# Kernel optimization log

Measured on AMD Instinct MI355X. Metric: run time of the kernel, lower is better.

The kernel has to match this reference:

```python
import jax, jax.numpy as jnp
import numpy as np

EPS = 1e-12  # torch F.normalize eps

def _l2norm(v, axis):
    n = jnp.sqrt(jnp.sum(v * v, axis=axis, keepdims=True))
    return v / jnp.maximum(n, EPS)

def setup_inputs() -> dict:
    key = jax.random.key(0)
    ks = jax.random.split(key, 5)
    B, N, C, K = 16, 512, 384, 64
    return {
        "x": jax.random.normal(ks[0], (B, N, C), dtype=jnp.float32),
        "centers": jax.random.normal(ks[1], (C, K), dtype=jnp.float32),
        "tran_ms": jax.random.normal(ks[2], (K, N, N), dtype=jnp.float32),
        "proj_w": jax.random.normal(ks[3], (C, C), dtype=jnp.float32) * 0.02,
        "proj_b": jax.random.normal(ks[4], (C,), dtype=jnp.float32) * 0.02,
    }

def reference(x, centers, tran_ms, proj_w, proj_b):
    # x: [B,N,C]
    q = x.mean(axis=1)                              # [B,C] mean-pooled query
    qn = _l2norm(q, axis=-1)                        # F.normalize(q, dim=-1)
    cn = _l2norm(centers, axis=0)                   # F.normalize(centers, dim=0)
    attn = jax.nn.softmax(qn @ cn, axis=-1)         # [B,K] cluster routing weights
    # combine transition matrices: equivalent to the (B,K,N,N) repeat/sum,
    # expressed as a single contraction producing [B,N,N]
    tm = jnp.einsum('bk,knm->bnm', attn, tran_ms)   # [B,N,N]
    y = jnp.einsum('bnm,bmc->bnc', tm, x)           # bmm
    out = y @ proj_w.T + proj_b                     # nn.Linear(dim, dim)
    return out
```

## Files before the change

### kernel.cpp

```cpp
#include <hip/hip_runtime.h>
#include <math.h>
#include <stdint.h>

#define B_  16
#define N_  512
#define C_  384
#define K_  64
#define NN_ (N_*N_)

typedef short bf16x8 __attribute__((ext_vector_type(8)));
typedef float f32x4  __attribute__((ext_vector_type(4)));

__device__ __forceinline__ unsigned short f2bf(float f) {
    union { float f; unsigned u; } v; v.f = f;
    unsigned r = v.u + 0x7FFF + ((v.u >> 16) & 1);
    return (unsigned short)(r >> 16);
}

__device__ __forceinline__ void gl_lds16(const void* g, void* l) {
    __builtin_amdgcn_global_load_lds(
        (const __attribute__((address_space(1))) unsigned*)g,
        (__attribute__((address_space(3))) unsigned*)l, 16, 0, 0);
}

__global__ __launch_bounds__(384) void mean_kernel(const float* __restrict__ x,
                                                   float* __restrict__ q,
                                                   unsigned short* __restrict__ xb) {
    const int b = blockIdx.y;
    const int s = blockIdx.x;
    const int c = threadIdx.x;
    const size_t base = ((size_t)(b * N_ + s * 16)) * C_ + c;
    const float* xp = x + base;
    unsigned short* xo = xb + base;
    float acc = 0.f;
#pragma unroll
    for (int i = 0; i < 16; ++i) {
        float v = xp[(size_t)i * C_];
        acc += v;
        xo[(size_t)i * C_] = f2bf(v);
    }
    atomicAdd(&q[b * C_ + c], acc);
}

__global__ __launch_bounds__(256) void wconv_kernel(const float* __restrict__ w,
                                                    unsigned short* __restrict__ wb) {
    const int i = (blockIdx.x * 256 + threadIdx.x) * 4;
    const float4 v = *(const float4*)(w + i);
    unsigned u0 = ((unsigned)f2bf(v.y) << 16) | f2bf(v.x);
    unsigned u1 = ((unsigned)f2bf(v.w) << 16) | f2bf(v.z);
    *(uint2*)(wb + i) = make_uint2(u0, u1);
}

__global__ __launch_bounds__(64) void attn_kernel(const float* __restrict__ q,
                                                  const float* __restrict__ centers,
                                                  float* __restrict__ attn) {
    const int b = blockIdx.x;
    const int k = threadIdx.x;
    const float* qb = q + b * C_;

    float qn2 = 0.f;
    for (int c = k; c < C_; c += 64) { float v = qb[c]; qn2 += v * v; }
#pragma unroll
    for (int off = 32; off > 0; off >>= 1) qn2 += __shfl_xor(qn2, off);
    const float qnorm = fmaxf(sqrtf(qn2), 1e-12f);

    float dot = 0.f, cn2 = 0.f;
    for (int c = 0; c < C_; ++c) {
        float sv = centers[c * K_ + k];
        float qc = qb[c];
        dot = fmaf(qc, sv, dot);
        cn2 = fmaf(sv, sv, cn2);
    }
    const float logit = dot / (qnorm * fmaxf(sqrtf(cn2), 1e-12f));

    float m = logit;
#pragma unroll
    for (int off = 32; off > 0; off >>= 1) m = fmaxf(m, __shfl_xor(m, off));
    const float e = expf(logit - m);
    float ssum = e;
#pragma unroll
    for (int off = 32; off > 0; off >>= 1) ssum += __shfl_xor(ssum, off);
    attn[b * K_ + k] = e / ssum;
}

__global__ __launch_bounds__(256) void tm_kernel(const float* __restrict__ tran,
                                                 const float* __restrict__ attn,
                                                 unsigned short* __restrict__ tmb) {
    __shared__ float a_s[B_ * K_];
    const int tid = threadIdx.x;
    for (int i = tid; i < B_ * K_; i += 256) a_s[i] = attn[i];
    __syncthreads();

    const size_t j = ((size_t)blockIdx.x * 256 + tid) * 4;
    float4 acc[B_];
#pragma unroll
    for (int b = 0; b < B_; ++b) acc[b] = make_float4(0.f, 0.f, 0.f, 0.f);

    for (int k = 0; k < K_; ++k) {
        const float4 t = *(const float4*)(tran + (size_t)k * NN_ + j);
#pragma unroll
        for (int b = 0; b < B_; ++b) {
            float s = a_s[b * K_ + k];
            acc[b].x = fmaf(s, t.x, acc[b].x);
            acc[b].y = fmaf(s, t.y, acc[b].y);
            acc[b].z = fmaf(s, t.z, acc[b].z);
            acc[b].w = fmaf(s, t.w, acc[b].w);
        }
    }
#pragma unroll
    for (int b = 0; b < B_; ++b) {
        unsigned u0 = ((unsigned)f2bf(acc[b].y) << 16) | f2bf(acc[b].x);
        unsigned u1 = ((unsigned)f2bf(acc[b].w) << 16) | f2bf(acc[b].z);
        *(uint2*)(tmb + (size_t)b * NN_ + j) = make_uint2(u0, u1);
    }
}

__global__ __launch_bounds__(256) void xw_mfma(const unsigned short* __restrict__ Xb,
                                               const unsigned short* __restrict__ Wb,
                                               unsigned short* __restrict__ xwT) {
    __shared__ unsigned short As[64 * 64];
    __shared__ unsigned short Bs[64 * 64];
    __shared__ float T[4][32 * 35];

    const int tid  = threadIdx.x;
    const int row0 = blockIdx.x * 64;
    const int col0 = blockIdx.y * 64;
    const int lane = tid & 63;
    const int w    = tid >> 6;
    const int wm   = w & 1, wn = w >> 1;
    const int quad = lane >> 4, l15 = lane & 15;

    const int sm = tid >> 3;
    const int sc = tid & 7;

    f32x4 acc[2][2] = {};

    for (int k0 = 0; k0 < C_; k0 += 64) {
        __syncthreads();
#pragma unroll
        for (int p = 0; p < 2; ++p) {
            const int m  = p * 32 + sm;
            const int gc = sc ^ (m & 7);
            gl_lds16(Xb + (size_t)(row0 + m) * C_ + k0 + gc * 8,
                     As + (p * 256 + tid) * 8);
            gl_lds16(Wb + (size_t)(col0 + m) * C_ + k0 + gc * 8,
                     Bs + (p * 256 + tid) * 8);
        }
        __syncthreads();
#pragma unroll
        for (int kk = 0; kk < 2; ++kk) {
            bf16x8 afr[2], bfr[2];
#pragma unroll
            for (int mt = 0; mt < 2; ++mt) {
                const int mr = wm * 32 + mt * 16 + l15;
                const int kc = (kk * 4 + quad) ^ (mr & 7);
                afr[mt] = *(const bf16x8*)(As + mr * 64 + kc * 8);
            }
#pragma unroll
            for (int nt = 0; nt < 2; ++nt) {
                const int nr = wn * 32 + nt * 16 + l15;
                const int kc = (kk * 4 + quad) ^ (nr & 7);
                bfr[nt] = *(const bf16x8*)(Bs + nr * 64 + kc * 8);
            }
#pragma unroll
            for (int mt = 0; mt < 2; ++mt)
#pragma unroll
                for (int nt = 0; nt < 2; ++nt)
                    acc[mt][nt] = __builtin_amdgcn_mfma_f32_16x16x32_bf16(
                        afr[mt], bfr[nt], acc[mt][nt], 0, 0, 0);
        }
    }

#pragma unroll
    for (int mt = 0; mt < 2; ++mt)
#pragma unroll
        for (int nt = 0; nt < 2; ++nt)
#pragma unroll
            for (int r = 0; r < 4; ++r) {
                const int lrow = mt * 16 + quad * 4 + r;
                const int lcol = nt * 16 + l15;
                T[w][lrow * 35 + lcol] = acc[mt][nt][r];
            }
    __syncthreads();

    const int rw = row0 + wm * 32;
    const int b  = rw >> 9;
    const int m0 = rw & 511;
    const int c0 = col0 + wn * 32;
    unsigned short* dst = xwT + (size_t)b * C_ * N_;
#pragma unroll
    for (int i = 0; i < 8; ++i) {
        const int cl = i * 4 + quad;
        const int ml = l15 * 2;
        const float v0 = T[w][(ml + 0) * 35 + cl];
        const float v1 = T[w][(ml + 1) * 35 + cl];
        const unsigned u = ((unsigned)f2bf(v1) << 16) | f2bf(v0);
        *(unsigned*)(dst + (size_t)(c0 + cl) * N_ + m0 + ml) = u;
    }
}

__global__ __launch_bounds__(256) void out_mfma(const unsigned short* __restrict__ Ab,
                                                const unsigned short* __restrict__ Bt,
                                                const float* __restrict__ bias,
                                                float* __restrict__ out) {
    __shared__ unsigned short As[64 * 64];
    __shared__ unsigned short Bs[64 * 64];

    const int tid  = threadIdx.x;
    const int b    = blockIdx.z;
    const int row0 = blockIdx.x * 64;
    const int col0 = blockIdx.y * 64;
    const int lane = tid & 63;
    const int w    = tid >> 6;
    const int wm   = w & 1, wn = w >> 1;
    const int quad = lane >> 4, l15 = lane & 15;

    const unsigned short* Abase = Ab + (size_t)b * N_ * N_;
    const unsigned short* Bbase = Bt + (size_t)b * C_ * N_;

    const int sm = tid >> 3;
    const int sc = tid & 7;

    f32x4 acc[2][2] = {};

    for (int k0 = 0; k0 < N_; k0 += 64) {
        __syncthreads();
#pragma unroll
        for (int p = 0; p < 2; ++p) {
            const int m  = p * 32 + sm;
            const int gc = sc ^ (m & 7);
            gl_lds16(Abase + (size_t)(row0 + m) * N_ + k0 + gc * 8,
                     As + (p * 256 + tid) * 8);
            gl_lds16(Bbase + (size_t)(col0 + m) * N_ + k0 + gc * 8,
                     Bs + (p * 256 + tid) * 8);
        }
        __syncthreads();
#pragma unroll
        for (int kk = 0; kk < 2; ++kk) {
            bf16x8 afr[2], bfr[2];
#pragma unroll
            for (int mt = 0; mt < 2; ++mt) {
                const int mr = wm * 32 + mt * 16 + l15;
                const int kc = (kk * 4 + quad) ^ (mr & 7);
                afr[mt] = *(const bf16x8*)(As + mr * 64 + kc * 8);
            }
#pragma unroll
            for (int nt = 0; nt < 2; ++nt) {
                const int nr = wn * 32 + nt * 16 + l15;
                const int kc = (kk * 4 + quad) ^ (nr & 7);
                bfr[nt] = *(const bf16x8*)(Bs + nr * 64 + kc * 8);
            }
#pragma unroll
            for (int mt = 0; mt < 2; ++mt)
#pragma unroll
                for (int nt = 0; nt < 2; ++nt)
                    acc[mt][nt] = __builtin_amdgcn_mfma_f32_16x16x32_bf16(
                        afr[mt], bfr[nt], acc[mt][nt], 0, 0, 0);
        }
    }

#pragma unroll
    for (int nt = 0; nt < 2; ++nt) {
        const int c  = col0 + wn * 32 + nt * 16 + l15;
        const float bv = bias[c];
#pragma unroll
        for (int mt = 0; mt < 2; ++mt) {
            const int rbase = row0 + wm * 32 + mt * 16 + quad * 4;
#pragma unroll
            for (int r = 0; r < 4; ++r)
                out[((size_t)(b * N_ + rbase + r)) * C_ + c] = acc[mt][nt][r] + bv;
        }
    }
}

extern "C" void kernel_launch(void* const* d_in, const int* in_sizes, int n_in,
                              void* d_out, int out_size, void* d_ws, size_t ws_size,
                              hipStream_t stream) {
    const float* x       = (const float*)d_in[0];
    const float* centers = (const float*)d_in[1];
    const float* tran    = (const float*)d_in[2];
    const float* proj_w  = (const float*)d_in[3];
    const float* proj_b  = (const float*)d_in[4];
    float* out = (float*)d_out;

    float* ws   = (float*)d_ws;
    float* q    = ws;
    float* attn = ws + 6144;
    unsigned short* tmb = (unsigned short*)(ws + 8192);
    unsigned short* xwT = tmb + (size_t)B_ * N_ * N_;
    unsigned short* xb  = xwT + (size_t)B_ * C_ * N_;
    unsigned short* wb  = xb  + (size_t)B_ * N_ * C_;

    hipMemsetAsync(q, 0, (size_t)B_ * C_ * sizeof(float), stream);

    mean_kernel<<<dim3(32, 16), 384, 0, stream>>>(x, q, xb);
    wconv_kernel<<<144, 256, 0, stream>>>(proj_w, wb);
    attn_kernel<<<16, 64, 0, stream>>>(q, centers, attn);
    tm_kernel<<<256, 256, 0, stream>>>(tran, attn, tmb);
    xw_mfma<<<dim3(128, 6), 256, 0, stream>>>(xb, wb, xwT);
    out_mfma<<<dim3(8, 6, 16), 256, 0, stream>>>(tmb, xwT, proj_b, out);
}
```

Before: 158.9 us.

## Drop memset and weight-convert launches; deterministic mean partials; vectorize tm weights

Replaces atomic accumulation of the mean with per-slice partial sums that attn_kernel reduces itself, which removes the memset launch and the atomics. Removes wconv_kernel by converting proj_w to bf16 inside xw_mfma during staging, using register loads and LDS stores in place of the async global-to-LDS copy. Transposes the attention weights in LDS so tm_kernel reads four weights per float4 load. Fewer launches cut fixed overhead, but xw_mfma now reads fp32 weights repeatedly and converts them per tile.

```diff
diff --git a/kernel.cpp b/kernel.cpp
--- a/kernel.cpp
+++ b/kernel.cpp
@@ -16,6 +16,9 @@
     unsigned r = v.u + 0x7FFF + ((v.u >> 16) & 1);
     return (unsigned short)(r >> 16);
 }
+__device__ __forceinline__ unsigned pack2(float a, float b) {
+    return ((unsigned)f2bf(b) << 16) | f2bf(a);
+}
 
 __device__ __forceinline__ void gl_lds16(const void* g, void* l) {
     __builtin_amdgcn_global_load_lds(
@@ -23,8 +26,15 @@
         (__attribute__((address_space(3))) unsigned*)l, 16, 0, 0);
 }
 
+__device__ __forceinline__ void fma4(float4& c, float s, const float4& v) {
+    c.x = fmaf(s, v.x, c.x);
+    c.y = fmaf(s, v.y, c.y);
+    c.z = fmaf(s, v.z, c.z);
+    c.w = fmaf(s, v.w, c.w);
+}
+
 __global__ __launch_bounds__(384) void mean_kernel(const float* __restrict__ x,
-                                                   float* __restrict__ q,
+                                                   float* __restrict__ part,
                                                    unsigned short* __restrict__ xb) {
     const int b = blockIdx.y;
     const int s = blockIdx.x;
@@ -39,56 +49,60 @@
         acc += v;
         xo[(size_t)i * C_] = f2bf(v);
     }
-    atomicAdd(&q[b * C_ + c], acc);
-}
-
-__global__ __launch_bounds__(256) void wconv_kernel(const float* __restrict__ w,
-                                                    unsigned short* __restrict__ wb) {
-    const int i = (blockIdx.x * 256 + threadIdx.x) * 4;
-    const float4 v = *(const float4*)(w + i);
-    unsigned u0 = ((unsigned)f2bf(v.y) << 16) | f2bf(v.x);
-    unsigned u1 = ((unsigned)f2bf(v.w) << 16) | f2bf(v.z);
-    *(uint2*)(wb + i) = make_uint2(u0, u1);
-}
-
-__global__ __launch_bounds__(64) void attn_kernel(const float* __restrict__ q,
-                                                  const float* __restrict__ centers,
-                                                  float* __restrict__ attn) {
+    part[((size_t)b * 32 + s) * C_ + c] = acc;
+}
+
+__global__ __launch_bounds__(384) void attn_kernel(const float* __restrict__ part,
+                                                   const float* __restrict__ centers,
+                                                   float* __restrict__ attn) {
+    __shared__ float q_lds[C_];
+    __shared__ float red[6];
     const int b = blockIdx.x;
-    const int k = threadIdx.x;
-    const float* qb = q + b * C_;
-
-    float qn2 = 0.f;
-    for (int c = k; c < C_; c += 64) { float v = qb[c]; qn2 += v * v; }
-#pragma unroll
-    for (int off = 32; off > 0; off >>= 1) qn2 += __shfl_xor(qn2, off);
-    const float qnorm = fmaxf(sqrtf(qn2), 1e-12f);
-
-    float dot = 0.f, cn2 = 0.f;
-    for (int c = 0; c < C_; ++c) {
-        float sv = centers[c * K_ + k];
-        float qc = qb[c];
-        dot = fmaf(qc, sv, dot);
-        cn2 = fmaf(sv, sv, cn2);
-    }
-    const float logit = dot / (qnorm * fmaxf(sqrtf(cn2), 1e-12f));
-
-    float m = logit;
-#pragma unroll
-    for (int off = 32; off > 0; off >>= 1) m = fmaxf(m, __shfl_xor(m, off));
-    const float e = expf(logit - m);
-    float ssum = e;
-#pragma unroll
-    for (int off = 32; off > 0; off >>= 1) ssum += __shfl_xor(ssum, off);
-    attn[b * K_ + k] = e / ssum;
+    const int tid = threadIdx.x;
+
+    const float* pb = part + (size_t)b * 32 * C_ + tid;
+    float s = 0.f;
+#pragma unroll
+    for (int i = 0; i < 32; ++i) s += pb[(size_t)i * C_];
+    q_lds[tid] = s;
+    float p2 = s * s;
+#pragma unroll
+    for (int off = 32; off > 0; off >>= 1) p2 += __shfl_xor(p2, off);
+    if ((tid & 63) == 0) red[tid >> 6] = p2;
+    __syncthreads();
+
+    if (tid < 64) {
+        const int k = tid;
+        const float qn2 = red[0] + red[1] + red[2] + red[3] + red[4] + red[5];
+        const float qnorm = fmaxf(sqrtf(qn2), 1e-12f);
+
+        float dot = 0.f, cn2 = 0.f;
+        for (int c = 0; c < C_; ++c) {
+            float sv = centers[c * K_ + k];
+            float qc = q_lds[c];
+            dot = fmaf(qc, sv, dot);
+            cn2 = fmaf(sv, sv, cn2);
+        }
+        const float logit = dot / (qnorm * fmaxf(sqrtf(cn2), 1e-12f));
+
+        float m = logit;
+#pragma unroll
+        for (int off = 32; off > 0; off >>= 1) m = fmaxf(m, __shfl_xor(m, off));
+        const float e = expf(logit - m);
+        float ssum = e;
+#pragma unroll
+        for (int off = 32; off > 0; off >>= 1) ssum += __shfl_xor(ssum, off);
+        attn[b * K_ + k] = e / ssum;
+    }
 }
 
 __global__ __launch_bounds__(256) void tm_kernel(const float* __restrict__ tran,
                                                  const float* __restrict__ attn,
                                                  unsigned short* __restrict__ tmb) {
-    __shared__ float a_s[B_ * K_];
+    __shared__ float a_s[K_ * B_];
     const int tid = threadIdx.x;
-    for (int i = tid; i < B_ * K_; i += 256) a_s[i] = attn[i];
+    for (int i = tid; i < K_ * B_; i += 256)
+        a_s[i] = attn[(i & 15) * K_ + (i >> 4)];
     __syncthreads();
 
     const size_t j = ((size_t)blockIdx.x * 256 + tid) * 4;
@@ -98,25 +112,26 @@
 
     for (int k = 0; k < K_; ++k) {
         const float4 t = *(const float4*)(tran + (size_t)k * NN_ + j);
-#pragma unroll
-        for (int b = 0; b < B_; ++b) {
-            float s = a_s[b * K_ + k];
-            acc[b].x = fmaf(s, t.x, acc[b].x);
-            acc[b].y = fmaf(s, t.y, acc[b].y);
-            acc[b].z = fmaf(s, t.z, acc[b].z);
-            acc[b].w = fmaf(s, t.w, acc[b].w);
-        }
+        const float4* wp = (const float4*)(a_s + k * 16);
+        const float4 w0 = wp[0], w1 = wp[1], w2 = wp[2], w3 = wp[3];
+        fma4(acc[0],  w0.x, t); fma4(acc[1],  w0.y, t);
+        fma4(acc[2],  w0.z, t); fma4(acc[3],  w0.w, t);
+        fma4(acc[4],  w1.x, t); fma4(acc[5],  w1.y, t);
+        fma4(acc[6],  w1.z, t); fma4(acc[7],  w1.w, t);
+        fma4(acc[8],  w2.x, t); fma4(acc[9],  w2.y, t);
+        fma4(acc[10], w2.z, t); fma4(acc[11], w2.w, t);
+        fma4(acc[12], w3.x, t); fma4(acc[13], w3.y, t);
+        fma4(acc[14], w3.z, t); fma4(acc[15], w3.w, t);
     }
 #pragma unroll
     for (int b = 0; b < B_; ++b) {
-        unsigned u0 = ((unsigned)f2bf(acc[b].y) << 16) | f2bf(acc[b].x);
-        unsigned u1 = ((unsigned)f2bf(acc[b].w) << 16) | f2bf(acc[b].z);
-        *(uint2*)(tmb + (size_t)b * NN_ + j) = make_uint2(u0, u1);
+        *(uint2*)(tmb + (size_t)b * NN_ + j) =
+            make_uint2(pack2(acc[b].x, acc[b].y), pack2(acc[b].z, acc[b].w));
     }
 }
 
 __global__ __launch_bounds__(256) void xw_mfma(const unsigned short* __restrict__ Xb,
-                                               const unsigned short* __restrict__ Wb,
+                                               const float* __restrict__ Wf,
                                                unsigned short* __restrict__ xwT) {
     __shared__ unsigned short As[64 * 64];
     __shared__ unsigned short Bs[64 * 64];
@@ -136,6 +151,15 @@
     f32x4 acc[2][2] = {};
 
     for (int k0 = 0; k0 < C_; k0 += 64) {
+        float4 wv[2][2];
+#pragma unroll
+        for (int p = 0; p < 2; ++p) {
+            const int m  = p * 32 + sm;
+            const int gc = sc ^ (m & 7);
+            const float* src = Wf + (size_t)(col0 + m) * C_ + k0 + gc * 8;
+            wv[p][0] = *(const float4*)(src);
+            wv[p][1] = *(const float4*)(src + 4);
+        }
         __syncthreads();
 #pragma unroll
         for (int p = 0; p < 2; ++p) {
@@ -143,8 +167,11 @@
             const int gc = sc ^ (m & 7);
             gl_lds16(Xb + (size_t)(row0 + m) * C_ + k0 + gc * 8,
                      As + (p * 256 + tid) * 8);
-            gl_lds16(Wb + (size_t)(col0 + m) * C_ + k0 + gc * 8,
-                     Bs + (p * 256 + tid) * 8);
+            const uint4 u = make_uint4(pack2(wv[p][0].x, wv[p][0].y),
+                                       pack2(wv[p][0].z, wv[p][0].w),
+                                       pack2(wv[p][1].x, wv[p][1].y),
+                                       pack2(wv[p][1].z, wv[p][1].w));
+            *(uint4*)(Bs + (p * 256 + tid) * 8) = u;
         }
         __syncthreads();
 #pragma unroll
@@ -176,11 +203,8 @@
 #pragma unroll
         for (int nt = 0; nt < 2; ++nt)
 #pragma unroll
-            for (int r = 0; r < 4; ++r) {
-                const int lrow = mt * 16 + quad * 4 + r;
-                const int lcol = nt * 16 + l15;
-                T[w][lrow * 35 + lcol] = acc[mt][nt][r];
-            }
+            for (int r = 0; r < 4; ++r)
+                T[w][(mt * 16 + quad * 4 + r) * 35 + nt * 16 + l15] = acc[mt][nt][r];
     __syncthreads();
 
     const int rw = row0 + wm * 32;
@@ -194,8 +218,7 @@
         const int ml = l15 * 2;
         const float v0 = T[w][(ml + 0) * 35 + cl];
         const float v1 = T[w][(ml + 1) * 35 + cl];
-        const unsigned u = ((unsigned)f2bf(v1) << 16) | f2bf(v0);
-        *(unsigned*)(dst + (size_t)(c0 + cl) * N_ + m0 + ml) = u;
+        *(unsigned*)(dst + (size_t)(c0 + cl) * N_ + m0 + ml) = pack2(v0, v1);
     }
 }
 
@@ -284,19 +307,15 @@
     float* out = (float*)d_out;
 
     float* ws   = (float*)d_ws;
-    float* q    = ws;
-    float* attn = ws + 6144;
-    unsigned short* tmb = (unsigned short*)(ws + 8192);
+    float* part = ws;
+    float* attn = ws + 196608;
+    unsigned short* tmb = (unsigned short*)(ws + 197632);
     unsigned short* xwT = tmb + (size_t)B_ * N_ * N_;
     unsigned short* xb  = xwT + (size_t)B_ * C_ * N_;
-    unsigned short* wb  = xb  + (size_t)B_ * N_ * C_;
-
-    hipMemsetAsync(q, 0, (size_t)B_ * C_ * sizeof(float), stream);
-
-    mean_kernel<<<dim3(32, 16), 384, 0, stream>>>(x, q, xb);
-    wconv_kernel<<<144, 256, 0, stream>>>(proj_w, wb);
-    attn_kernel<<<16, 64, 0, stream>>>(q, centers, attn);
+
+    mean_kernel<<<dim3(32, 16), 384, 0, stream>>>(x, part, xb);
+    attn_kernel<<<16, 384, 0, stream>>>(part, centers, attn);
     tm_kernel<<<256, 256, 0, stream>>>(tran, attn, tmb);
-    xw_mfma<<<dim3(128, 6), 256, 0, stream>>>(xb, wb, xwT);
+    xw_mfma<<<dim3(128, 6), 256, 0, stream>>>(xb, proj_w, xwT);
     out_mfma<<<dim3(8, 6, 16), 256, 0, stream>>>(tmb, xwT, proj_b, out);
 }
```

After: 163.5 us. 2.9% more time.
